# Kernel tuning notes

Hardware: AMD Instinct MI355X
Metric: run time of the kernel (lower is better)

The kernel has to match this reference:

```python
import jax, jax.numpy as jnp
import numpy as np

EMBED_DIM = 512
NUM_HEADS = 8
HEAD_DIM = EMBED_DIM // NUM_HEADS
FACTOR = 5
B, T = 4, 2048


def setup_inputs() -> dict:
    key = jax.random.key(0)
    ks = jax.random.split(key, 10)
    s = EMBED_DIM ** -0.5
    hidden_states = jax.random.normal(ks[0], (B, T, EMBED_DIM), dtype=jnp.float32)
    log_L = int(np.ceil(np.log1p(T)))
    u_part = min(FACTOR * T * log_L, T)
    index_sample = jax.random.randint(ks[1], (u_part,), 0, T, dtype=jnp.int32)
    Wq = jax.random.normal(ks[2], (EMBED_DIM, EMBED_DIM), dtype=jnp.float32) * s
    bq = jnp.zeros((EMBED_DIM,), dtype=jnp.float32)
    Wk = jax.random.normal(ks[3], (EMBED_DIM, EMBED_DIM), dtype=jnp.float32) * s
    bk = jnp.zeros((EMBED_DIM,), dtype=jnp.float32)
    Wv = jax.random.normal(ks[4], (EMBED_DIM, EMBED_DIM), dtype=jnp.float32) * s
    bv = jnp.zeros((EMBED_DIM,), dtype=jnp.float32)
    Wo = jax.random.normal(ks[5], (EMBED_DIM, EMBED_DIM), dtype=jnp.float32) * s
    bo = jnp.zeros((EMBED_DIM,), dtype=jnp.float32)
    return {"hidden_states": hidden_states, "index_sample": index_sample,
            "Wq": Wq, "bq": bq, "Wk": Wk, "bk": bk, "Wv": Wv, "bv": bv,
            "Wo": Wo, "bo": bo}


def _split_heads(x, bsz, seqlen):
    # [B, T, E] -> [B*H, T, head_dim]
    return x.reshape(bsz, seqlen, NUM_HEADS, HEAD_DIM).transpose(0, 2, 1, 3).reshape(bsz * NUM_HEADS, seqlen, HEAD_DIM)


def reference(hidden_states, index_sample, Wq, bq, Wk, bk, Wv, bv, Wo, bo):
    bsz, tgt_len, embed_dim = hidden_states.shape
    scaling = HEAD_DIM ** -0.5
    q = (hidden_states @ Wq.T + bq) * scaling
    k = hidden_states @ Wk.T + bk
    v = hidden_states @ Wv.T + bv
    q = _split_heads(q, bsz, tgt_len)   # [BH, T, d]
    k = _split_heads(k, bsz, tgt_len)
    v = _split_heads(v, bsz, tgt_len)
    L_k = tgt_len
    log_q = int(np.ceil(np.log1p(tgt_len)))
    u = min(FACTOR * log_q, tgt_len)
    # random key sampling (indices precomputed, length u_part)
    k_sample = k[:, index_sample, :]                                  # [BH, u_part, d]
    qk_sample = jnp.einsum('bqd,bkd->bqk', q, k_sample)               # [BH, T, u_part]
    # sparsity measurement: max - mean over sampled keys (mean uses full L_k as in source)
    sparsity = qk_sample.max(axis=-1) - qk_sample.sum(axis=-1) / L_k  # [BH, T]
    top_idx = jax.lax.top_k(sparsity, u)[1]                           # [BH, u]
    q_reduce = jnp.take_along_axis(q, top_idx[:, :, None], axis=1)    # [BH, u, d]
    attn = jax.nn.softmax(jnp.einsum('bud,bkd->buk', q_reduce, k), axis=-1)  # [BH, u, L]
    attn_out = jnp.einsum('buk,bkd->bud', attn, v)                    # [BH, u, d]
    # encoder context: mean of values over time, scattered with active-query outputs
    context = jnp.broadcast_to(v.mean(axis=1, keepdims=True), v.shape)  # [BH, T, d]
    bh_idx = jnp.arange(bsz * NUM_HEADS)[:, None]
    context = context.at[bh_idx, top_idx].set(attn_out)
    out = context.reshape(bsz, NUM_HEADS, tgt_len, HEAD_DIM).transpose(0, 2, 1, 3).reshape(bsz, tgt_len, embed_dim)
    return out @ Wo.T + bo
```

## Files before the change

kernel.cpp:

```cpp
#include <hip/hip_runtime.h>
#include <hip/hip_bf16.h>
#include <math.h>

#define T_LEN 2048
#define EMB   512
#define NHEAD 8
#define HDIM  64
#define BHEADS 32
#define USEL  40

typedef __bf16 bf16v8 __attribute__((ext_vector_type(8)));
typedef _Float16 f16x8 __attribute__((ext_vector_type(8)));
typedef float f32x4 __attribute__((ext_vector_type(4)));
typedef unsigned short u16;

__device__ __forceinline__ void cvt4_hilo(const float4 f, uint2& ph, uint2& pl)
{
    __hip_bfloat16 h0 = __float2bfloat16(f.x);
    __hip_bfloat16 h1 = __float2bfloat16(f.y);
    __hip_bfloat16 h2 = __float2bfloat16(f.z);
    __hip_bfloat16 h3 = __float2bfloat16(f.w);
    __hip_bfloat16 l0 = __float2bfloat16(f.x - __bfloat162float(h0));
    __hip_bfloat16 l1 = __float2bfloat16(f.y - __bfloat162float(h1));
    __hip_bfloat16 l2 = __float2bfloat16(f.z - __bfloat162float(h2));
    __hip_bfloat16 l3 = __float2bfloat16(f.w - __bfloat162float(h3));
    ph.x = (unsigned)*(const u16*)&h0 | ((unsigned)*(const u16*)&h1 << 16);
    ph.y = (unsigned)*(const u16*)&h2 | ((unsigned)*(const u16*)&h3 << 16);
    pl.x = (unsigned)*(const u16*)&l0 | ((unsigned)*(const u16*)&l1 << 16);
    pl.y = (unsigned)*(const u16*)&l2 | ((unsigned)*(const u16*)&l3 << 16);
}

__device__ __forceinline__ void cvt4_hilo_h(const float4 f, uint2& ph, uint2& pl)
{
    _Float16 h0 = (_Float16)f.x;
    _Float16 h1 = (_Float16)f.y;
    _Float16 h2 = (_Float16)f.z;
    _Float16 h3 = (_Float16)f.w;
    _Float16 l0 = (_Float16)(f.x - (float)h0);
    _Float16 l1 = (_Float16)(f.y - (float)h1);
    _Float16 l2 = (_Float16)(f.z - (float)h2);
    _Float16 l3 = (_Float16)(f.w - (float)h3);
    ph.x = (unsigned)*(const u16*)&h0 | ((unsigned)*(const u16*)&h1 << 16);
    ph.y = (unsigned)*(const u16*)&h2 | ((unsigned)*(const u16*)&h3 << 16);
    pl.x = (unsigned)*(const u16*)&l0 | ((unsigned)*(const u16*)&l1 << 16);
    pl.y = (unsigned)*(const u16*)&l2 | ((unsigned)*(const u16*)&l3 << 16);
}

__global__ __launch_bounds__(256)
void pack_hilo_kernel(const float* __restrict__ X,
                      const float* __restrict__ Wq, const float* __restrict__ Wk,
                      const float* __restrict__ Wv,
                      u16* __restrict__ Xp, u16* __restrict__ Wp)
{
    alignas(16) __shared__ u16 th[4096];
    alignas(16) __shared__ u16 tl[4096];
    const int b = blockIdx.x, tid = threadIdx.x;

    const float* src; u16* dst;
    if (b < 1024) {
        int mt = b >> 4, kt = b & 15;
        src = X + (size_t)(mt * 128) * EMB + kt * 32;
        dst = Xp + (size_t)b * 8192;
    } else {
        int wdx = b - 1024;
        int z = wdx >> 6, nt = (wdx >> 4) & 3, kt = wdx & 15;
        const float* W = (z == 0) ? Wq : (z == 1) ? Wk : Wv;
        src = W + (size_t)(nt * 128) * EMB + kt * 32;
        dst = Wp + (size_t)wdx * 8192;
    }

    #pragma unroll
    for (int s = 0; s < 4; ++s) {
        int u = tid + 256 * s;
        int row = u >> 3, c4 = u & 7;
        float4 f = *(const float4*)&src[(size_t)row * EMB + c4 * 4];
        uint2 ph, pl;
        cvt4_hilo_h(f, ph, pl);
        int kq = c4 >> 1, e4 = (c4 & 1) * 4;
        *(uint2*)&th[kq * 1024 + row * 8 + e4] = ph;
        *(uint2*)&tl[kq * 1024 + row * 8 + e4] = pl;
    }
    __syncthreads();

    uint4* d4 = (uint4*)dst;
    const uint4* s4h = (const uint4*)th;
    const uint4* s4l = (const uint4*)tl;
    d4[tid]       = s4h[tid];
    d4[tid + 256] = s4h[tid + 256];
    d4[tid + 512] = s4l[tid];
    d4[tid + 768] = s4l[tid + 256];
}

__global__ __launch_bounds__(256)
void qkv_mfma_kernel(const u16* __restrict__ Xp, const u16* __restrict__ Wp,
                     const float* __restrict__ bq, const float* __restrict__ bk,
                     const float* __restrict__ bv,
                     float* __restrict__ qo, float* __restrict__ ko, float* __restrict__ vo)
{
    alignas(16) __shared__ u16 Ah[2][4096];
    alignas(16) __shared__ u16 Al[2][4096];
    alignas(16) __shared__ u16 Bh[2][4096];
    alignas(16) __shared__ u16 Bl[2][4096];

    const int z = blockIdx.z;
    const float* bias; float* dst; float scale;
    if (z == 0)      { bias = bq; dst = qo; scale = 0.125f; }
    else if (z == 1) { bias = bk; dst = ko; scale = 1.0f;   }
    else             { bias = bv; dst = vo; scale = 1.0f;   }
    const bool three = (z != 2);

    const int tid = threadIdx.x;
    const int mt = blockIdx.x;
    const int nt = blockIdx.y;
    const int w = tid >> 6, lane = tid & 63;
    const int wm = w & 1, wn = w >> 1;
    const int lm = lane & 15, kq = lane >> 4;

    const u16* Abase = Xp + (size_t)mt * (16 * 8192);
    const u16* Bbase = Wp + (size_t)(z * 4 + nt) * (16 * 8192);

    f32x4 acc[4][4];
    #pragma unroll
    for (int i = 0; i < 4; ++i)
        #pragma unroll
        for (int j = 0; j < 4; ++j)
            #pragma unroll
            for (int r = 0; r < 4; ++r) acc[i][j][r] = 0.0f;

    auto stage = [&](int kt, int buf) {
        const u16* at = Abase + kt * 8192;
        const u16* bt = Bbase + kt * 8192;
        const u16* gsrc; u16* ldst;
        if (w == 0)      { gsrc = at;        ldst = &Ah[buf][0]; }
        else if (w == 1) { gsrc = at + 4096; ldst = &Al[buf][0]; }
        else if (w == 2) { gsrc = bt;        ldst = &Bh[buf][0]; }
        else             { gsrc = bt + 4096; ldst = &Bl[buf][0]; }
        if (three || (w & 1) == 0) {
            #pragma unroll
            for (int i = 0; i < 8; ++i)
                __builtin_amdgcn_global_load_lds(
                    (const __attribute__((address_space(1))) void*)(gsrc + (size_t)lane * 8 + i * 512),
                    (__attribute__((address_space(3))) void*)(ldst + i * 512),
                    16, 0, 0);
        }
    };

    stage(0, 0);

    for (int kt = 0; kt < 16; ++kt) {
        const int cur = kt & 1;
        if (kt + 1 < 16) {
            stage(kt + 1, cur ^ 1);
            asm volatile("s_waitcnt vmcnt(8)" ::: "memory");
        } else {
            asm volatile("s_waitcnt vmcnt(0)" ::: "memory");
        }
        __builtin_amdgcn_s_barrier();
        __builtin_amdgcn_sched_barrier(0);

        f16x8 ah[4], al[4], bh[4], bl[4];
        #pragma unroll
        for (int i = 0; i < 4; ++i) {
            int ar = (wm * 64 + i * 16 + lm) * 8 + kq * 1024;
            int br = (wn * 64 + i * 16 + lm) * 8 + kq * 1024;
            ah[i] = *(const f16x8*)&Ah[cur][ar];
            bh[i] = *(const f16x8*)&Bh[cur][br];
            if (three) {
                al[i] = *(const f16x8*)&Al[cur][ar];
                bl[i] = *(const f16x8*)&Bl[cur][br];
            }
        }
        #pragma unroll
        for (int i = 0; i < 4; ++i)
            #pragma unroll
            for (int j = 0; j < 4; ++j) {
                acc[i][j] = __builtin_amdgcn_mfma_f32_16x16x32_f16(ah[i], bh[j], acc[i][j], 0, 0, 0);
                if (three) {
                    acc[i][j] = __builtin_amdgcn_mfma_f32_16x16x32_f16(ah[i], bl[j], acc[i][j], 0, 0, 0);
                    acc[i][j] = __builtin_amdgcn_mfma_f32_16x16x32_f16(al[i], bh[j], acc[i][j], 0, 0, 0);
                }
            }
        __builtin_amdgcn_s_barrier();
    }

    #pragma unroll
    for (int j = 0; j < 4; ++j) {
        int ng = nt * 128 + wn * 64 + j * 16 + lm;
        int h = ng >> 6, d = ng & 63;
        float bv_ = bias[ng];
        #pragma unroll
        for (int i = 0; i < 4; ++i) {
            #pragma unroll
            for (int r = 0; r < 4; ++r) {
                int mg = mt * 128 + wm * 64 + i * 16 + kq * 4 + r;
                int b = mg >> 11, t = mg & 2047;
                dst[((size_t)((b * NHEAD + h) * T_LEN + t)) * HDIM + d] =
                    (acc[i][j][r] + bv_) * scale;
            }
        }
    }
}

__global__ __launch_bounds__(256)
void qkv_proj_kernel(const float* __restrict__ X,
                     const float* __restrict__ Wq, const float* __restrict__ bq,
                     const float* __restrict__ Wk, const float* __restrict__ bk,
                     const float* __restrict__ Wv, const float* __restrict__ bv,
                     float* __restrict__ qo, float* __restrict__ ko, float* __restrict__ vo)
{
    alignas(16) __shared__ u16 Ah[128 * 40];
    alignas(16) __shared__ u16 Al[128 * 40];
    alignas(16) __shared__ u16 Bh[128 * 40];
    alignas(16) __shared__ u16 Bl[128 * 40];

    const int z = blockIdx.z;
    const float* W; const float* bias; float* dst; float scale;
    if (z == 0)      { W = Wq; bias = bq; dst = qo; scale = 0.125f; }
    else if (z == 1) { W = Wk; bias = bk; dst = ko; scale = 1.0f;   }
    else             { W = Wv; bias = bv; dst = vo; scale = 1.0f;   }

    const int tid = threadIdx.x;
    const int m0 = blockIdx.x * 128;
    const int n0 = blockIdx.y * 128;
    const int w = tid >> 6, lane = tid & 63;
    const int wm = w & 1, wn = w >> 1;
    const int lm = lane & 15, kq = lane >> 4;

    f32x4 acc[4][4];
    #pragma unroll
    for (int i = 0; i < 4; ++i)
        #pragma unroll
        for (int j = 0; j < 4; ++j)
            #pragma unroll
            for (int r = 0; r < 4; ++r) acc[i][j][r] = 0.0f;

    for (int kc = 0; kc < EMB; kc += 32) {
        __syncthreads();
        #pragma unroll
        for (int s = 0; s < 4; ++s) {
            int u = tid + 256 * s;
            int row = u >> 3, c4 = u & 7;
            float4 fa = *(const float4*)&X[(size_t)(m0 + row) * EMB + kc + c4 * 4];
            float4 fb = *(const float4*)&W[(n0 + row) * EMB + kc + c4 * 4];
            uint2 ph, pl;
            cvt4_hilo_h(fa, ph, pl);
            *(uint2*)&Ah[row * 40 + c4 * 4] = ph;
            *(uint2*)&Al[row * 40 + c4 * 4] = pl;
            cvt4_hilo_h(fb, ph, pl);
            *(uint2*)&Bh[row * 40 + c4 * 4] = ph;
            *(uint2*)&Bl[row * 40 + c4 * 4] = pl;
        }
        __syncthreads();

        f16x8 ah[4], al[4], bh[4], bl[4];
        #pragma unroll
        for (int i = 0; i < 4; ++i) {
            int ra = (wm * 64 + i * 16 + lm) * 40 + kq * 8;
            ah[i] = *(const f16x8*)&Ah[ra];
            al[i] = *(const f16x8*)&Al[ra];
            int rb = (wn * 64 + i * 16 + lm) * 40 + kq * 8;
            bh[i] = *(const f16x8*)&Bh[rb];
            bl[i] = *(const f16x8*)&Bl[rb];
        }
        #pragma unroll
        for (int i = 0; i < 4; ++i)
            #pragma unroll
            for (int j = 0; j < 4; ++j) {
                acc[i][j] = __builtin_amdgcn_mfma_f32_16x16x32_f16(ah[i], bh[j], acc[i][j], 0, 0, 0);
                acc[i][j] = __builtin_amdgcn_mfma_f32_16x16x32_f16(ah[i], bl[j], acc[i][j], 0, 0, 0);
                acc[i][j] = __builtin_amdgcn_mfma_f32_16x16x32_f16(al[i], bh[j], acc[i][j], 0, 0, 0);
            }
    }

    #pragma unroll
    for (int j = 0; j < 4; ++j) {
        int ng = n0 + wn * 64 + j * 16 + lm;
        int h = ng >> 6, d = ng & 63;
        float bv_ = bias[ng];
        #pragma unroll
        for (int i = 0; i < 4; ++i) {
            #pragma unroll
            for (int r = 0; r < 4; ++r) {
                int mg = m0 + wm * 64 + i * 16 + kq * 4 + r;
                int b = mg >> 11, t = mg & 2047;
                dst[((size_t)((b * NHEAD + h) * T_LEN + t)) * HDIM + d] =
                    (acc[i][j][r] + bv_) * scale;
            }
        }
    }
}

__global__ __launch_bounds__(256)
void count_compact_kernel(const int* __restrict__ idxs, int n,
                          int* __restrict__ count, int* __restrict__ klist,
                          int* __restrict__ ncp)
{
    __shared__ int cnt[T_LEN];
    __shared__ int th_tot[256];
    __shared__ int th_off[256];
    __shared__ int ncs;
    const int tid = threadIdx.x;
    for (int j = tid; j < T_LEN; j += 256) cnt[j] = 0;
    __syncthreads();
    for (int i = tid; i < n; i += 256) atomicAdd(&cnt[idxs[i] & (T_LEN - 1)], 1);
    __syncthreads();
    const int base = tid * 8;
    int flags[8]; int loc = 0;
    #pragma unroll
    for (int j = 0; j < 8; ++j) {
        int c = cnt[base + j];
        count[base + j] = c;
        flags[j] = (c > 0); loc += flags[j];
    }
    th_tot[tid] = loc;
    __syncthreads();
    if (tid == 0) {
        int run = 0;
        for (int i = 0; i < 256; ++i) { th_off[i] = run; run += th_tot[i]; }
        ncs = run;
        ncp[0] = run;
    }
    __syncthreads();
    int off = th_off[tid];
    #pragma unroll
    for (int j = 0; j < 8; ++j)
        if (flags[j]) klist[off++] = base + j;
    __syncthreads();
    const int nc = ncs;
    const int nt = (nc + 127) & ~127;
    const int k0 = klist[0];
    for (int j = nc + tid; j < nt; j += 256) klist[j] = k0;
}

__global__ __launch_bounds__(256)
void ksum_vmean_part_kernel(const int* __restrict__ count,
                            const float* __restrict__ k, const float* __restrict__ v,
                            float* __restrict__ kpart, float* __restrict__ vpart)
{
    __shared__ int cs[256];
    alignas(16) __shared__ float rk[16 * 64];
    alignas(16) __shared__ float rv[16 * 64];

    const int sl = blockIdx.x, bh = blockIdx.y, tid = threadIdx.x;
    const int f4 = tid & 15, tg = tid >> 4;
    const int t0 = sl * 256;

    cs[tid] = count[t0 + tid];
    __syncthreads();

    const float4* k4 = (const float4*)(k + (size_t)bh * T_LEN * HDIM) + t0 * 16;
    const float4* v4 = (const float4*)(v + (size_t)bh * T_LEN * HDIM) + t0 * 16;

    float4 ak = {0.f, 0.f, 0.f, 0.f}, av = {0.f, 0.f, 0.f, 0.f};
    #pragma unroll
    for (int s = 0; s < 16; ++s) {
        int t = tg + s * 16;
        float c = (float)cs[t];
        float4 kf = k4[t * 16 + f4];
        float4 vf = v4[t * 16 + f4];
        ak.x = fmaf(c, kf.x, ak.x); ak.y = fmaf(c, kf.y, ak.y);
        ak.z = fmaf(c, kf.z, ak.z); ak.w = fmaf(c, kf.w, ak.w);
        av.x += vf.x; av.y += vf.y; av.z += vf.z; av.w += vf.w;
    }
    *(float4*)&rk[tg * 64 + f4 * 4] = ak;
    *(float4*)&rv[tg * 64 + f4 * 4] = av;
    __syncthreads();

    if (tid < 64) {
        float sk = 0.f, sv = 0.f;
        #pragma unroll
        for (int g = 0; g < 16; ++g) { sk += rk[g * 64 + tid]; sv += rv[g * 64 + tid]; }
        kpart[((size_t)bh * 8 + sl) * 64 + tid] = sk;
        vpart[((size_t)bh * 8 + sl) * 64 + tid] = sv;
    }
}

__global__ __launch_bounds__(64)
void ksum_vmean_reduce_kernel(const float* __restrict__ kpart, const float* __restrict__ vpart,
                              float* __restrict__ ksum, float* __restrict__ vmean)
{
    const int bh = blockIdx.x, d = threadIdx.x;
    float sk = 0.f, sv = 0.f;
    #pragma unroll
    for (int sl = 0; sl < 8; ++sl) {
        sk += kpart[((size_t)bh * 8 + sl) * 64 + d];
        sv += vpart[((size_t)bh * 8 + sl) * 64 + d];
    }
    ksum[bh * 64 + d]  = sk;
    vmean[bh * 64 + d] = sv * (1.0f / 2048.0f);
}

__global__ __launch_bounds__(256)
void pack_k_kernel(const float* __restrict__ k, const int* __restrict__ klist,
                   const int* __restrict__ ncp, u16* __restrict__ Kp)
{
    alignas(16) __shared__ u16 th[8192];
    alignas(16) __shared__ u16 tl[8192];
    const int wg = blockIdx.x, tid = threadIdx.x;
    const int swz = (wg & 7) * 64 + (wg >> 3);
    const int bh = swz >> 4, kt = swz & 15;
    const int ntiles = (ncp[0] + 127) >> 7;
    if (kt >= ntiles) return;

    const float4* kb4 = (const float4*)(k + (size_t)bh * T_LEN * HDIM);
    #pragma unroll
    for (int s = 0; s < 8; ++s) {
        int u = tid + 256 * s;
        int row = u >> 4, c4 = u & 15;
        int krow = klist[kt * 128 + row];
        float4 f = kb4[krow * 16 + c4];
        uint2 ph, pl;
        cvt4_hilo_h(f, ph, pl);
        int base = (c4 >> 3) * 4096 + ((c4 >> 1) & 3) * 1024 + row * 8 + (c4 & 1) * 4;
        *(uint2*)&th[base] = ph;
        *(uint2*)&tl[base] = pl;
    }
    __syncthreads();

    u16* dst = Kp + ((size_t)bh * 16 + kt) * 16384;
    uint4* d4 = (uint4*)dst;
    const uint4* s4h = (const uint4*)th;
    const uint4* s4l = (const uint4*)tl;
    #pragma unroll
    for (int i = 0; i < 4; ++i) d4[tid + 256 * i] = s4h[tid + 256 * i];
    #pragma unroll
    for (int i = 0; i < 4; ++i) d4[1024 + tid + 256 * i] = s4l[tid + 256 * i];
}

__global__ __launch_bounds__(256)
void sparsity_scan_kernel(const float* __restrict__ q, const u16* __restrict__ Kp,
                          const float* __restrict__ ksum,
                          const int* __restrict__ ncp, float* __restrict__ spars)
{
    alignas(16) __shared__ u16 KH[10240];
    alignas(16) __shared__ u16 KL[10240];
    __shared__ float ksm[64];
    __shared__ float smax[128];
    __shared__ float sdotL[128];

    const int tid = threadIdx.x;
    const int wg = blockIdx.x;
    const int swz = (wg & 7) * 64 + (wg >> 3);
    const int bh = swz >> 4;
    const int q0 = (swz & 15) * 128;
    const int w = tid >> 6, lane = tid & 63;
    const int lm = lane & 15, kq = lane >> 4;

    const float* qb = q + ((size_t)bh * T_LEN + q0) * HDIM;
    const int ntiles = (ncp[0] + 127) >> 7;

    if (tid < 64) ksm[tid] = ksum[bh * 64 + tid];

    #pragma unroll
    for (int s = 0; s < 8; ++s) {
        int u = tid + 256 * s;
        int row = u >> 4, c4 = u & 15;
        float4 f = *(const float4*)&qb[row * HDIM + c4 * 4];
        uint2 ph, pl;
        cvt4_hilo_h(f, ph, pl);
        int base = ((c4 >> 3) * 128 + row) * 40 + (c4 & 7) * 4;
        *(uint2*)&KH[base] = ph;
        *(uint2*)&KL[base] = pl;
    }
    __syncthreads();

    f16x8 qh[2][2], ql[2][2];
    #pragma unroll
    for (int i = 0; i < 2; ++i)
        #pragma unroll
        for (int c = 0; c < 2; ++c) {
            int ra = (c * 128 + w * 32 + i * 16 + lm) * 40 + kq * 8;
            qh[i][c] = *(const f16x8*)&KH[ra];
            ql[i][c] = *(const f16x8*)&KL[ra];
        }

    {
        float4 k0a = *(const float4*)&ksm[kq * 8];
        float4 k0b = *(const float4*)&ksm[kq * 8 + 4];
        float4 k1a = *(const float4*)&ksm[32 + kq * 8];
        float4 k1b = *(const float4*)&ksm[32 + kq * 8 + 4];
        float kmv[2][8] = {{k0a.x, k0a.y, k0a.z, k0a.w, k0b.x, k0b.y, k0b.z, k0b.w},
                           {k1a.x, k1a.y, k1a.z, k1a.w, k1b.x, k1b.y, k1b.z, k1b.w}};
        #pragma unroll
        for (int i = 0; i < 2; ++i) {
            float sd = 0.f;
            #pragma unroll
            for (int c = 0; c < 2; ++c)
                #pragma unroll
                for (int e = 0; e < 8; ++e)
                    sd = fmaf((float)qh[i][c][e] + (float)ql[i][c][e], kmv[c][e], sd);
            sd += __shfl_xor(sd, 16, 64);
            sd += __shfl_xor(sd, 32, 64);
            if (kq == 0) sdotL[w * 32 + i * 16 + lm] = sd;
        }
    }

    float vmax[2][4];
    #pragma unroll
    for (int i = 0; i < 2; ++i)
        #pragma unroll
        for (int r = 0; r < 4; ++r) vmax[i][r] = -INFINITY;

    const u16* kpb = Kp + (size_t)bh * (16 * 16384);

    for (int kt = 0; kt < ntiles; ++kt) {
        __syncthreads();
        const u16* kp = kpb + kt * 16384;
        const u16* gsrc; u16* ldst;
        if (w == 0)      { gsrc = kp;         ldst = KH; }
        else if (w == 1) { gsrc = kp + 4096;  ldst = KH + 4096; }
        else if (w == 2) { gsrc = kp + 8192;  ldst = KL; }
        else             { gsrc = kp + 12288; ldst = KL + 4096; }
        #pragma unroll
        for (int i = 0; i < 8; ++i)
            __builtin_amdgcn_global_load_lds(
                (const __attribute__((address_space(1))) void*)(gsrc + (size_t)lane * 8 + i * 512),
                (__attribute__((address_space(3))) void*)(ldst + i * 512),
                16, 0, 0);
        __syncthreads();

        #pragma unroll
        for (int j = 0; j < 8; ++j) {
            int rb0 = kq * 1024 + (j * 16 + lm) * 8;
            int rb1 = 4096 + kq * 1024 + (j * 16 + lm) * 8;
            f16x8 bh0 = *(const f16x8*)&KH[rb0];
            f16x8 bl0 = *(const f16x8*)&KL[rb0];
            f16x8 bh1 = *(const f16x8*)&KH[rb1];
            f16x8 bl1 = *(const f16x8*)&KL[rb1];
            f32x4 a0 = {0.f, 0.f, 0.f, 0.f};
            f32x4 a1 = {0.f, 0.f, 0.f, 0.f};
            a0 = __builtin_amdgcn_mfma_f32_16x16x32_f16(qh[0][0], bh0, a0, 0, 0, 0);
            a1 = __builtin_amdgcn_mfma_f32_16x16x32_f16(qh[1][0], bh0, a1, 0, 0, 0);
            a0 = __builtin_amdgcn_mfma_f32_16x16x32_f16(qh[0][0], bl0, a0, 0, 0, 0);
            a1 = __builtin_amdgcn_mfma_f32_16x16x32_f16(qh[1][0], bl0, a1, 0, 0, 0);
            a0 = __builtin_amdgcn_mfma_f32_16x16x32_f16(ql[0][0], bh0, a0, 0, 0, 0);
            a1 = __builtin_amdgcn_mfma_f32_16x16x32_f16(ql[1][0], bh0, a1, 0, 0, 0);
            a0 = __builtin_amdgcn_mfma_f32_16x16x32_f16(qh[0][1], bh1, a0, 0, 0, 0);
            a1 = __builtin_amdgcn_mfma_f32_16x16x32_f16(qh[1][1], bh1, a1, 0, 0, 0);
            a0 = __builtin_amdgcn_mfma_f32_16x16x32_f16(qh[0][1], bl1, a0, 0, 0, 0);
            a1 = __builtin_amdgcn_mfma_f32_16x16x32_f16(qh[1][1], bl1, a1, 0, 0, 0);
            a0 = __builtin_amdgcn_mfma_f32_16x16x32_f16(ql[0][1], bh1, a0, 0, 0, 0);
            a1 = __builtin_amdgcn_mfma_f32_16x16x32_f16(ql[1][1], bh1, a1, 0, 0, 0);
            #pragma unroll
            for (int r = 0; r < 4; ++r) {
                vmax[0][r] = fmaxf(vmax[0][r], a0[r]);
                vmax[1][r] = fmaxf(vmax[1][r], a1[r]);
            }
        }
    }

    #pragma unroll
    for (int i = 0; i < 2; ++i)
        #pragma unroll
        for (int r = 0; r < 4; ++r) {
            float m = vmax[i][r];
            m = fmaxf(m, __shfl_xor(m, 1, 64));
            m = fmaxf(m, __shfl_xor(m, 2, 64));
            m = fmaxf(m, __shfl_xor(m, 4, 64));
            m = fmaxf(m, __shfl_xor(m, 8, 64));
            if (lm == 0) smax[w * 32 + i * 16 + kq * 4 + r] = m;
        }
    __syncthreads();

    if (tid < 128)
        spars[bh * T_LEN + q0 + tid] = smax[tid] - sdotL[tid] * (1.0f / 2048.0f);
}

__global__ __launch_bounds__(256)
void sparsity_scan_fb_kernel(const float* __restrict__ q, const float* __restrict__ k,
                             const float* __restrict__ ksum, const int* __restrict__ klist,
                             const int* __restrict__ ncp, float* __restrict__ spars)
{
    alignas(16) __shared__ u16 KH[256 * 40];
    alignas(16) __shared__ u16 KL[256 * 40];
    __shared__ float ksm[64];
    __shared__ float smax[128];
    __shared__ float sdotL[128];

    const int tid = threadIdx.x;
    const int bh = blockIdx.y;
    const int q0 = blockIdx.x * 128;
    const int w = tid >> 6, lane = tid & 63;
    const int lm = lane & 15, kq = lane >> 4;

    const float* qb = q + ((size_t)bh * T_LEN + q0) * HDIM;
    const float4* kb4 = (const float4*)(k + (size_t)bh * T_LEN * HDIM);
    const int ntiles = (ncp[0] + 127) >> 7;

    if (tid < 64) ksm[tid] = ksum[bh * 64 + tid];

    #pragma unroll
    for (int s = 0; s < 8; ++s) {
        int u = tid + 256 * s;
        int row = u >> 4, c4 = u & 15;
        float4 f = *(const float4*)&qb[row * HDIM + c4 * 4];
        uint2 ph, pl;
        cvt4_hilo_h(f, ph, pl);
        int base = ((c4 >> 3) * 128 + row) * 40 + (c4 & 7) * 4;
        *(uint2*)&KH[base] = ph;
        *(uint2*)&KL[base] = pl;
    }
    __syncthreads();

    f16x8 qh[2][2], ql[2][2];
    #pragma unroll
    for (int i = 0; i < 2; ++i)
        #pragma unroll
        for (int c = 0; c < 2; ++c) {
            int ra = (c * 128 + w * 32 + i * 16 + lm) * 40 + kq * 8;
            qh[i][c] = *(const f16x8*)&KH[ra];
            ql[i][c] = *(const f16x8*)&KL[ra];
        }

    {
        float4 k0a = *(const float4*)&ksm[kq * 8];
        float4 k0b = *(const float4*)&ksm[kq * 8 + 4];
        float4 k1a = *(const float4*)&ksm[32 + kq * 8];
        float4 k1b = *(const float4*)&ksm[32 + kq * 8 + 4];
        float kmv[2][8] = {{k0a.x, k0a.y, k0a.z, k0a.w, k0b.x, k0b.y, k0b.z, k0b.w},
                           {k1a.x, k1a.y, k1a.z, k1a.w, k1b.x, k1b.y, k1b.z, k1b.w}};
        #pragma unroll
        for (int i = 0; i < 2; ++i) {
            float sd = 0.f;
            #pragma unroll
            for (int c = 0; c < 2; ++c)
                #pragma unroll
                for (int e = 0; e < 8; ++e)
                    sd = fmaf((float)qh[i][c][e] + (float)ql[i][c][e], kmv[c][e], sd);
            sd += __shfl_xor(sd, 16, 64);
            sd += __shfl_xor(sd, 32, 64);
            if (kq == 0) sdotL[w * 32 + i * 16 + lm] = sd;
        }
    }

    float vmax[2][4];
    #pragma unroll
    for (int i = 0; i < 2; ++i)
        #pragma unroll
        for (int r = 0; r < 4; ++r) vmax[i][r] = -INFINITY;

    for (int kt = 0; kt < ntiles; ++kt) {
        __syncthreads();
        #pragma unroll
        for (int s = 0; s < 8; ++s) {
            int u = tid + 256 * s;
            int row = u >> 4, c4 = u & 15;
            int krow = klist[kt * 128 + row];
            float4 f = kb4[krow * 16 + c4];
            uint2 ph, pl;
            cvt4_hilo_h(f, ph, pl);
            int base = ((c4 >> 3) * 128 + row) * 40 + (c4 & 7) * 4;
            *(uint2*)&KH[base] = ph;
            *(uint2*)&KL[base] = pl;
        }
        __syncthreads();

        #pragma unroll
        for (int j = 0; j < 8; ++j) {
            int rb0 = (j * 16 + lm) * 40 + kq * 8;
            int rb1 = (128 + j * 16 + lm) * 40 + kq * 8;
            f16x8 bh0 = *(const f16x8*)&KH[rb0];
            f16x8 bl0 = *(const f16x8*)&KL[rb0];
            f16x8 bh1 = *(const f16x8*)&KH[rb1];
            f16x8 bl1 = *(const f16x8*)&KL[rb1];
            f32x4 a0 = {0.f, 0.f, 0.f, 0.f};
            f32x4 a1 = {0.f, 0.f, 0.f, 0.f};
            a0 = __builtin_amdgcn_mfma_f32_16x16x32_f16(qh[0][0], bh0, a0, 0, 0, 0);
            a1 = __builtin_amdgcn_mfma_f32_16x16x32_f16(qh[1][0], bh0, a1, 0, 0, 0);
            a0 = __builtin_amdgcn_mfma_f32_16x16x32_f16(qh[0][0], bl0, a0, 0, 0, 0);
            a1 = __builtin_amdgcn_mfma_f32_16x16x32_f16(qh[1][0], bl0, a1, 0, 0, 0);
            a0 = __builtin_amdgcn_mfma_f32_16x16x32_f16(ql[0][0], bh0, a0, 0, 0, 0);
            a1 = __builtin_amdgcn_mfma_f32_16x16x32_f16(ql[1][0], bh0, a1, 0, 0, 0);
            a0 = __builtin_amdgcn_mfma_f32_16x16x32_f16(qh[0][1], bh1, a0, 0, 0, 0);
            a1 = __builtin_amdgcn_mfma_f32_16x16x32_f16(qh[1][1], bh1, a1, 0, 0, 0);
            a0 = __builtin_amdgcn_mfma_f32_16x16x32_f16(qh[0][1], bl1, a0, 0, 0, 0);
            a1 = __builtin_amdgcn_mfma_f32_16x16x32_f16(qh[1][1], bl1, a1, 0, 0, 0);
            a0 = __builtin_amdgcn_mfma_f32_16x16x32_f16(ql[0][1], bh1, a0, 0, 0, 0);
            a1 = __builtin_amdgcn_mfma_f32_16x16x32_f16(ql[1][1], bh1, a1, 0, 0, 0);
            #pragma unroll
            for (int r = 0; r < 4; ++r) {
                vmax[0][r] = fmaxf(vmax[0][r], a0[r]);
                vmax[1][r] = fmaxf(vmax[1][r], a1[r]);
            }
        }
    }

    #pragma unroll
    for (int i = 0; i < 2; ++i)
        #pragma unroll
        for (int r = 0; r < 4; ++r) {
            float m = vmax[i][r];
            m = fmaxf(m, __shfl_xor(m, 1, 64));
            m = fmaxf(m, __shfl_xor(m, 2, 64));
            m = fmaxf(m, __shfl_xor(m, 4, 64));
            m = fmaxf(m, __shfl_xor(m, 8, 64));
            if (lm == 0) smax[w * 32 + i * 16 + kq * 4 + r] = m;
        }
    __syncthreads();

    if (tid < 128)
        spars[bh * T_LEN + q0 + tid] = smax[tid] - sdotL[tid] * (1.0f / 2048.0f);
}

__global__ __launch_bounds__(256)
void topk_kernel(const float* __restrict__ spars, int* __restrict__ topi)
{
    __shared__ unsigned keys[T_LEN];
    __shared__ int hist[256];
    __shared__ int sfx[257];
    __shared__ int sh_need, sh_bin, nsel, neq, cnt2;
    const int bh = blockIdx.x, tid = threadIdx.x;

    #pragma unroll
    for (int s = 0; s < 8; ++s) {
        int j = tid + 256 * s;
        unsigned u = __float_as_uint(spars[bh * T_LEN + j]);
        keys[j] = (u & 0x80000000u) ? ~u : (u | 0x80000000u);
    }
    if (tid == 0) { sh_need = USEL; nsel = 0; neq = 0; cnt2 = 0; }
    __syncthreads();

    unsigned kpref = 0;
    int shift = 24;
    #pragma unroll
    for (int level = 0; level < 4; ++level) {
        const unsigned hi_mask = (shift == 24) ? 0u : (0xFFFFFFFFu << (shift + 8));
        hist[tid] = 0;
        __syncthreads();
        #pragma unroll
        for (int s = 0; s < 8; ++s) {
            unsigned kk = keys[tid + 256 * s];
            if ((kk & hi_mask) == kpref)
                atomicAdd(&hist[(kk >> shift) & 255], 1);
        }
        __syncthreads();
        sfx[tid] = hist[tid];
        if (tid == 0) sfx[256] = 0;
        __syncthreads();
        for (int off = 1; off < 256; off <<= 1) {
            int v = (tid + off < 256) ? sfx[tid + off] : 0;
            __syncthreads();
            sfx[tid] += v;
            __syncthreads();
        }
        const int need = sh_need;
        const int A = (tid == 255) ? 0 : sfx[tid + 1];
        const int here = sfx[tid];
        __syncthreads();
        if (A < need && here >= need) {
            sh_bin = tid;
            sh_need = need - A;
        }
        __syncthreads();
        kpref |= (unsigned)sh_bin << shift;
        shift -= 8;
    }

    const unsigned K = kpref;
    const int need_eq = sh_need;

    #pragma unroll
    for (int s = 0; s < 8; ++s) {
        int j = tid + 256 * s;
        unsigned kk = keys[j];
        if (kk > K) {
            int pos = atomicAdd(&nsel, 1);
            if (pos < USEL) topi[bh * USEL + pos] = j;
        } else if (kk == K) {
            atomicAdd(&neq, 1);
        }
    }
    __syncthreads();
    const int base = nsel;
    const int E = neq;
    __syncthreads();

    if (E == need_eq) {
        #pragma unroll
        for (int s = 0; s < 8; ++s) {
            int j = tid + 256 * s;
            if (keys[j] == K) {
                int pos = atomicAdd(&cnt2, 1);
                if (base + pos < USEL) topi[bh * USEL + base + pos] = j;
            }
        }
    } else {
        #pragma unroll
        for (int s = 0; s < 8; ++s) {
            int j = tid + 256 * s;
            if (keys[j] == K) {
                int rank = 0;
                for (int j2 = 0; j2 < j; ++j2) rank += (keys[j2] == K);
                if (rank < need_eq && base + rank < USEL)
                    topi[bh * USEL + base + rank] = j;
            }
        }
    }
}

__global__ __launch_bounds__(256)
void gather_q_kernel(const float* __restrict__ q, const int* __restrict__ topi,
                     float* __restrict__ qsel)
{
    const int bh = blockIdx.x, tid = threadIdx.x;
    for (int i = tid; i < USEL * HDIM; i += 256) {
        int u = i >> 6, d = i & 63;
        int t = topi[bh * USEL + u] & (T_LEN - 1);
        qsel[(size_t)bh * USEL * HDIM + i] = q[((size_t)bh * T_LEN + t) * HDIM + d];
    }
}

__global__ __launch_bounds__(256)
void sel_scores_kernel(const float* __restrict__ qsel, const float* __restrict__ k,
                       float* __restrict__ S)
{
    __shared__ float qsT[64 * 41];
    __shared__ float ksT[64 * 257];

    const int sl = blockIdx.x, bh = blockIdx.y, tid = threadIdx.x;
    const int t0 = sl * 256;

    for (int i = tid; i < USEL * HDIM; i += 256) {
        int u = i >> 6, d = i & 63;
        qsT[d * 41 + u] = qsel[(size_t)bh * USEL * HDIM + i];
    }
    const float4* k4 = (const float4*)(k + (size_t)bh * T_LEN * HDIM);
    #pragma unroll
    for (int s = 0; s < 16; ++s) {
        int u = tid + 256 * s;
        int c4 = u & 15, t = u >> 4;
        float4 f = k4[(t0 + t) * 16 + c4];
        ksT[(c4 * 4 + 0) * 257 + t] = f.x;
        ksT[(c4 * 4 + 1) * 257 + t] = f.y;
        ksT[(c4 * 4 + 2) * 257 + t] = f.z;
        ksT[(c4 * 4 + 3) * 257 + t] = f.w;
    }
    __syncthreads();

    const int qg = tid >> 5;
    const int kg = tid & 31;

    float acc[5][8];
    #pragma unroll
    for (int i = 0; i < 5; ++i)
        #pragma unroll
        for (int j = 0; j < 8; ++j) acc[i][j] = 0.0f;

    #pragma unroll 4
    for (int d = 0; d < 64; ++d) {
        float qv[5], kv[8];
        #pragma unroll
        for (int i = 0; i < 5; ++i) qv[i] = qsT[d * 41 + qg * 5 + i];
        #pragma unroll
        for (int j = 0; j < 8; ++j) kv[j] = ksT[d * 257 + kg + 32 * j];
        #pragma unroll
        for (int i = 0; i < 5; ++i)
            #pragma unroll
            for (int j = 0; j < 8; ++j)
                acc[i][j] = fmaf(qv[i], kv[j], acc[i][j]);
    }

    #pragma unroll
    for (int i = 0; i < 5; ++i) {
        float* sp = &S[((size_t)bh * USEL + qg * 5 + i) * T_LEN + t0 + kg];
        #pragma unroll
        for (int j = 0; j < 8; ++j) sp[32 * j] = acc[i][j];
    }
}

__global__ __launch_bounds__(256)
void sel_softmax_kernel(float* __restrict__ S)
{
    __shared__ float red[256];
    const int row = blockIdx.x, tid = threadIdx.x;
    float* sr = S + (size_t)row * T_LEN;

    float x[8];
    float m = -INFINITY;
    #pragma unroll
    for (int s = 0; s < 8; ++s) { x[s] = sr[tid + 256 * s]; m = fmaxf(m, x[s]); }
    red[tid] = m;
    __syncthreads();
    for (int s = 128; s > 0; s >>= 1) {
        if (tid < s) red[tid] = fmaxf(red[tid], red[tid + s]);
        __syncthreads();
    }
    m = red[0];
    __syncthreads();

    float sum = 0.f;
    #pragma unroll
    for (int s = 0; s < 8; ++s) { x[s] = __expf(x[s] - m); sum += x[s]; }
    red[tid] = sum;
    __syncthreads();
    for (int s = 128; s > 0; s >>= 1) {
        if (tid < s) red[tid] += red[tid + s];
        __syncthreads();
    }
    float inv = 1.0f / red[0];
    #pragma unroll
    for (int s = 0; s < 8; ++s) sr[tid + 256 * s] = x[s] * inv;
}

__global__ __launch_bounds__(256)
void pv_part_kernel(const float* __restrict__ S, const float* __restrict__ v,
                    float* __restrict__ part)
{
    __shared__ float ps[USEL * 128];
    __shared__ float vs[128 * 69];
    __shared__ float obuf[128 * 20];

    const int sl = blockIdx.x, bh = blockIdx.y, tid = threadIdx.x;
    const int t0 = sl * 128;

    for (int i = tid; i < USEL * 128; i += 256) {
        int q = i >> 7, t = i & 127;
        ps[q * 128 + t] = S[((size_t)bh * USEL + q) * T_LEN + t0 + t];
    }
    const float4* v4 = (const float4*)(v + (size_t)bh * T_LEN * HDIM);
    #pragma unroll
    for (int s = 0; s < 8; ++s) {
        int u = tid + 256 * s;
        int c4 = u & 15, t = u >> 4;
        float4 f = v4[(t0 + t) * 16 + c4];
        vs[t * 69 + c4 * 4 + 0] = f.x;
        vs[t * 69 + c4 * 4 + 1] = f.y;
        vs[t * 69 + c4 * 4 + 2] = f.z;
        vs[t * 69 + c4 * 4 + 3] = f.w;
    }
    __syncthreads();

    const int qg = tid >> 5, r = tid & 31;
    const int dg = r >> 1, th = r & 1;
    const int tb = th * 64;

    float o[5][4];
    #pragma unroll
    for (int i = 0; i < 5; ++i)
        #pragma unroll
        for (int j = 0; j < 4; ++j) o[i][j] = 0.0f;

    #pragma unroll 4
    for (int tt = 0; tt < 64; ++tt) {
        int t = tb + tt;
        float pv[5];
        #pragma unroll
        for (int i = 0; i < 5; ++i) pv[i] = ps[(qg * 5 + i) * 128 + t];
        float4 vv = *(const float4*)&vs[t * 69 + dg * 4];
        #pragma unroll
        for (int i = 0; i < 5; ++i) {
            o[i][0] = fmaf(pv[i], vv.x, o[i][0]);
            o[i][1] = fmaf(pv[i], vv.y, o[i][1]);
            o[i][2] = fmaf(pv[i], vv.z, o[i][2]);
            o[i][3] = fmaf(pv[i], vv.w, o[i][3]);
        }
    }

    const int p = qg * 16 + dg;
    if (th == 1) {
        #pragma unroll
        for (int i = 0; i < 5; ++i)
            #pragma unroll
            for (int j = 0; j < 4; ++j) obuf[p * 20 + i * 4 + j] = o[i][j];
    }
    __syncthreads();
    if (th == 0) {
        float* pb = part + ((size_t)bh * 16 + sl) * (USEL * HDIM);
        #pragma unroll
        for (int i = 0; i < 5; ++i)
            #pragma unroll
            for (int j = 0; j < 4; ++j)
                pb[(qg * 5 + i) * HDIM + dg * 4 + j] = o[i][j] + obuf[p * 20 + i * 4 + j];
    }
}

__global__ __launch_bounds__(256)
void pv_merge_kernel(const float* __restrict__ part, float* __restrict__ attn)
{
    const int bh = blockIdx.x, tid = threadIdx.x;
    for (int i = tid; i < USEL * HDIM; i += 256) {
        float s = 0.f;
        #pragma unroll
        for (int sl = 0; sl < 16; ++sl)
            s += part[((size_t)bh * 16 + sl) * (USEL * HDIM) + i];
        attn[(size_t)bh * USEL * HDIM + i] = s;
    }
}

__global__ __launch_bounds__(256)
void ctx_fill_kernel(const float* __restrict__ vmean, float* __restrict__ ctx)
{
    int flat = blockIdx.x * 256 + threadIdx.x;
    int d = flat & 63, h = (flat >> 6) & 7, b = flat >> 20;
    int bh = (b << 3) | h;
    ctx[flat] = vmean[bh * 64 + d];
}

__global__ void ctx_scatter_kernel(const float* __restrict__ attn, const int* __restrict__ topi,
                                   float* __restrict__ ctx)
{
    const int u = blockIdx.x, bh = blockIdx.y, d = threadIdx.x;
    const int b = bh >> 3, h = bh & 7;
    const int t = topi[bh * USEL + u] & (T_LEN - 1);
    ctx[(size_t)(b * T_LEN + t) * EMB + h * 64 + d] =
        attn[((size_t)bh * USEL + u) * HDIM + d];
}

__global__ __launch_bounds__(256)
void out_proj_kernel(const float* __restrict__ A, const float* __restrict__ Wo,
                     const float* __restrict__ bo, float* __restrict__ out)
{
    alignas(16) __shared__ u16 Ah[128 * 40];
    alignas(16) __shared__ u16 Al[128 * 40];
    alignas(16) __shared__ u16 Bh[128 * 40];
    alignas(16) __shared__ u16 Bl[128 * 40];

    const int tid = threadIdx.x;
    const int m0 = blockIdx.x * 128;
    const int n0 = blockIdx.y * 128;
    const int w = tid >> 6, lane = tid & 63;
    const int wm = w & 1, wn = w >> 1;
    const int lm = lane & 15, kq = lane >> 4;

    f32x4 acc[4][4];
    #pragma unroll
    for (int i = 0; i < 4; ++i)
        #pragma unroll
        for (int j = 0; j < 4; ++j)
            #pragma unroll
            for (int r = 0; r < 4; ++r) acc[i][j][r] = 0.0f;

    for (int kc = 0; kc < EMB; kc += 32) {
        __syncthreads();
        #pragma unroll
        for (int s = 0; s < 4; ++s) {
            int u = tid + 256 * s;
            int row = u >> 3, c4 = u & 7;
            float4 fa = *(const float4*)&A[(size_t)(m0 + row) * EMB + kc + c4 * 4];
            float4 fb = *(const float4*)&Wo[(n0 + row) * EMB + kc + c4 * 4];
            uint2 ph, pl;
            cvt4_hilo(fa, ph, pl);
            *(uint2*)&Ah[row * 40 + c4 * 4] = ph;
            *(uint2*)&Al[row * 40 + c4 * 4] = pl;
            cvt4_hilo(fb, ph, pl);
            *(uint2*)&Bh[row * 40 + c4 * 4] = ph;
            *(uint2*)&Bl[row * 40 + c4 * 4] = pl;
        }
        __syncthreads();

        bf16v8 ah[4], al[4], bh[4], bl[4];
        #pragma unroll
        for (int i = 0; i < 4; ++i) {
            int ra = (wm * 64 + i * 16 + lm) * 40 + kq * 8;
            ah[i] = *(const bf16v8*)&Ah[ra];
            al[i] = *(const bf16v8*)&Al[ra];
            int rb = (wn * 64 + i * 16 + lm) * 40 + kq * 8;
            bh[i] = *(const bf16v8*)&Bh[rb];
            bl[i] = *(const bf16v8*)&Bl[rb];
        }
        #pragma unroll
        for (int i = 0; i < 4; ++i)
            #pragma unroll
            for (int j = 0; j < 4; ++j) {
                acc[i][j] = __builtin_amdgcn_mfma_f32_16x16x32_bf16(ah[i], bh[j], acc[i][j], 0, 0, 0);
                acc[i][j] = __builtin_amdgcn_mfma_f32_16x16x32_bf16(ah[i], bl[j], acc[i][j], 0, 0, 0);
                acc[i][j] = __builtin_amdgcn_mfma_f32_16x16x32_bf16(al[i], bh[j], acc[i][j], 0, 0, 0);
            }
    }

    #pragma unroll
    for (int j = 0; j < 4; ++j) {
        int ng = n0 + wn * 64 + j * 16 + lm;
        float bias = bo[ng];
        #pragma unroll
        for (int i = 0; i < 4; ++i)
            #pragma unroll
            for (int r = 0; r < 4; ++r) {
                int mg = m0 + wm * 64 + i * 16 + kq * 4 + r;
                out[(size_t)mg * EMB + ng] = acc[i][j][r] + bias;
            }
    }
}

__global__ __launch_bounds__(256)
void ws_diag_kernel(float* __restrict__ out, int n, float mib)
{
    int flat = blockIdx.x * 256 + threadIdx.x;
    if (flat < n) out[flat] = mib;
}

extern "C" void kernel_launch(void* const* d_in, const int* in_sizes, int n_in,
                              void* d_out, int out_size, void* d_ws, size_t ws_size,
                              hipStream_t stream)
{
    const float* X = nullptr; const int* idxs = nullptr;
    const float* Wseen[4] = {nullptr, nullptr, nullptr, nullptr};
    const float* bseen[4] = {nullptr, nullptr, nullptr, nullptr};
    int nw = 0, nb = 0, u_part = 2048;
    for (int i = 0; i < n_in; ++i) {
        int sz = in_sizes[i];
        if (sz == EMB * EMB * 16) { if (!X) X = (const float*)d_in[i]; }
        else if (sz == T_LEN)     { if (!idxs) { idxs = (const int*)d_in[i]; u_part = sz; } }
        else if (sz == EMB * EMB) { if (nw < 4) Wseen[nw++] = (const float*)d_in[i]; }
        else if (sz == EMB)       { if (nb < 4) bseen[nb++] = (const float*)d_in[i]; }
    }
    if (!X || !idxs || nw < 4 || nb < 4) {
        X = (const float*)d_in[0]; idxs = (const int*)d_in[1];
        Wseen[0] = (const float*)d_in[2]; bseen[0] = (const float*)d_in[3];
        Wseen[1] = (const float*)d_in[4]; bseen[1] = (const float*)d_in[5];
        Wseen[2] = (const float*)d_in[6]; bseen[2] = (const float*)d_in[7];
        Wseen[3] = (const float*)d_in[8]; bseen[3] = (const float*)d_in[9];
        u_part = in_sizes[1];
    }
    const float *Wq = Wseen[0], *Wk = Wseen[1], *Wv = Wseen[2], *Wo = Wseen[3];
    const float *bq = bseen[0], *bk = bseen[1], *bv = bseen[2], *bo = bseen[3];

    const size_t NEED      = 50951168ULL;
    const size_t NEED_BIG  = NEED + 16777216ULL + 3145728ULL;
    if (ws_size < NEED) {
        ws_diag_kernel<<<(out_size + 255) / 256, 256, 0, stream>>>(
            (float*)d_out, out_size, (float)(ws_size >> 20));
        return;
    }

    float* ws    = (float*)d_ws;
    float* qw    = ws;
    float* kw    = qw + 4194304;
    float* vw    = kw + 4194304;
    float* tail  = vw + 4194304;
    float* slotA = tail;
    float* spars = tail + 81920;
    int*   count = (int*)(tail + 147456);
    float* ksum  = tail + 149504;
    float* vmean = tail + 151552;
    int*   topi  = (int*)(tail + 153600);
    float* kpart = tail;
    float* vpart = tail + 16384;
    int*   klist = (int*)(tail + 32768);
    int*   ncp   = (int*)(tail + 34816);
    float* S     = qw;
    float* pvp   = qw + 2621440;
    float* qsel  = slotA;
    float* attn  = slotA;
    float* ctx   = (float*)d_ws;
    u16*   Xp    = (u16*)((char*)d_ws + NEED);
    u16*   Wp    = Xp + 8388608;
    u16*   Kp    = Xp;

    const bool big = (ws_size >= NEED_BIG);

    if (big) {
        pack_hilo_kernel<<<1216, 256, 0, stream>>>(X, Wq, Wk, Wv, Xp, Wp);
        qkv_mfma_kernel<<<dim3(64, 4, 3), 256, 0, stream>>>(Xp, Wp, bq, bk, bv, qw, kw, vw);
    } else {
        qkv_proj_kernel<<<dim3(64, 4, 3), 256, 0, stream>>>(X, Wq, bq, Wk, bk, Wv, bv, qw, kw, vw);
    }
    count_compact_kernel<<<1, 256, 0, stream>>>(idxs, u_part, count, klist, ncp);
    ksum_vmean_part_kernel<<<dim3(8, 32), 256, 0, stream>>>(count, kw, vw, kpart, vpart);
    ksum_vmean_reduce_kernel<<<32, 64, 0, stream>>>(kpart, vpart, ksum, vmean);
    if (big) {
        pack_k_kernel<<<512, 256, 0, stream>>>(kw, klist, ncp, Kp);
        sparsity_scan_kernel<<<512, 256, 0, stream>>>(qw, Kp, ksum, ncp, spars);
    } else {
        sparsity_scan_fb_kernel<<<dim3(16, 32), 256, 0, stream>>>(qw, kw, ksum, klist, ncp, spars);
    }
    topk_kernel<<<32, 256, 0, stream>>>(spars, topi);
    gather_q_kernel<<<32, 256, 0, stream>>>(qw, topi, qsel);
    sel_scores_kernel<<<dim3(8, 32), 256, 0, stream>>>(qsel, kw, S);
    sel_softmax_kernel<<<1280, 256, 0, stream>>>(S);
    pv_part_kernel<<<dim3(16, 32), 256, 0, stream>>>(S, vw, pvp);
    pv_merge_kernel<<<32, 256, 0, stream>>>(pvp, attn);
    ctx_fill_kernel<<<16384, 256, 0, stream>>>(vmean, ctx);
    ctx_scatter_kernel<<<dim3(USEL, BHEADS), 64, 0, stream>>>(attn, topi, ctx);
    out_proj_kernel<<<dim3(64, 4), 256, 0, stream>>>(ctx, Wo, bo, (float*)d_out);
}
```

Measured before the change: 277.0 us.

## Run output projection on split-fp16 MFMA with pre-packed context tiles

```diff
diff --git a/kernel.cpp b/kernel.cpp
--- a/kernel.cpp
+++ b/kernel.cpp
@@ -46,10 +46,18 @@
     pl.y = (unsigned)*(const u16*)&l2 | ((unsigned)*(const u16*)&l3 << 16);
 }
 
+__device__ __forceinline__ void cvt1_hilo_h(float f, u16& h, u16& l)
+{
+    _Float16 hh = (_Float16)f;
+    _Float16 ll = (_Float16)(f - (float)hh);
+    h = *(const u16*)&hh;
+    l = *(const u16*)&ll;
+}
+
 __global__ __launch_bounds__(256)
 void pack_hilo_kernel(const float* __restrict__ X,
                       const float* __restrict__ Wq, const float* __restrict__ Wk,
-                      const float* __restrict__ Wv,
+                      const float* __restrict__ Wv, const float* __restrict__ Wo,
                       u16* __restrict__ Xp, u16* __restrict__ Wp)
 {
     alignas(16) __shared__ u16 th[4096];
@@ -64,7 +72,7 @@
     } else {
         int wdx = b - 1024;
         int z = wdx >> 6, nt = (wdx >> 4) & 3, kt = wdx & 15;
-        const float* W = (z == 0) ? Wq : (z == 1) ? Wk : Wv;
+        const float* W = (z == 0) ? Wq : (z == 1) ? Wk : (z == 2) ? Wv : Wo;
         src = W + (size_t)(nt * 128) * EMB + kt * 32;
         dst = Wp + (size_t)wdx * 8192;
     }
@@ -988,6 +996,152 @@
 }
 
 __global__ __launch_bounds__(256)
+void ctx_fill_pack_kernel(const float* __restrict__ vmean, u16* __restrict__ CXp)
+{
+    const int tile = blockIdx.x;
+    const int tid = threadIdx.x;
+    const int mt = tile >> 4, kt = tile & 15;
+    const int bh = ((mt >> 4) << 3) | (kt >> 1);
+    const int dbase = (kt & 1) * 32;
+
+    uint4 vh[4], vl[4];
+    #pragma unroll
+    for (int kq = 0; kq < 4; ++kq) {
+        unsigned hw[4], lw[4];
+        #pragma unroll
+        for (int p = 0; p < 4; ++p) {
+            u16 h0, l0, h1, l1;
+            cvt1_hilo_h(vmean[bh * 64 + dbase + kq * 8 + p * 2],     h0, l0);
+            cvt1_hilo_h(vmean[bh * 64 + dbase + kq * 8 + p * 2 + 1], h1, l1);
+            hw[p] = (unsigned)h0 | ((unsigned)h1 << 16);
+            lw[p] = (unsigned)l0 | ((unsigned)l1 << 16);
+        }
+        vh[kq] = make_uint4(hw[0], hw[1], hw[2], hw[3]);
+        vl[kq] = make_uint4(lw[0], lw[1], lw[2], lw[3]);
+    }
+
+    u16* dst = CXp + (size_t)tile * 8192;
+    uint4* dh = (uint4*)dst;
+    uint4* dl = (uint4*)(dst + 4096);
+    #pragma unroll
+    for (int s = 0; s < 2; ++s) {
+        int u = tid + 256 * s;
+        dh[u] = vh[u >> 7];
+        dl[u] = vl[u >> 7];
+    }
+}
+
+__global__ void ctx_scatter_pack_kernel(const float* __restrict__ attn,
+                                        const int* __restrict__ topi,
+                                        u16* __restrict__ CXp)
+{
+    const int u = blockIdx.x, bh = blockIdx.y, d = threadIdx.x;
+    const int b = bh >> 3, h = bh & 7;
+    const int t = topi[bh * USEL + u] & (T_LEN - 1);
+    const int m = b * T_LEN + t;
+    const int mt = m >> 7, row = m & 127;
+    const int e = h * 64 + d;
+    const int kt = e >> 5;
+    const int c = e & 31, kq = c >> 3, i = c & 7;
+    u16 hh, ll;
+    cvt1_hilo_h(attn[((size_t)bh * USEL + u) * HDIM + d], hh, ll);
+    u16* base = CXp + (size_t)(mt * 16 + kt) * 8192 + kq * 1024 + row * 8 + i;
+    base[0]    = hh;
+    base[4096] = ll;
+}
+
+__global__ __launch_bounds__(256)
+void out_mfma_kernel(const u16* __restrict__ CXp, const u16* __restrict__ Wp,
+                     const float* __restrict__ bo, float* __restrict__ out)
+{
+    alignas(16) __shared__ u16 Ah[2][4096];
+    alignas(16) __shared__ u16 Al[2][4096];
+    alignas(16) __shared__ u16 Bh[2][4096];
+    alignas(16) __shared__ u16 Bl[2][4096];
+
+    const int tid = threadIdx.x;
+    const int mt = blockIdx.x;
+    const int nt = blockIdx.y;
+    const int w = tid >> 6, lane = tid & 63;
+    const int wm = w & 1, wn = w >> 1;
+    const int lm = lane & 15, kq = lane >> 4;
+
+    const u16* Abase = CXp + (size_t)mt * (16 * 8192);
+    const u16* Bbase = Wp + (size_t)(3 * 4 + nt) * (16 * 8192);
+
+    f32x4 acc[4][4];
+    #pragma unroll
+    for (int i = 0; i < 4; ++i)
+        #pragma unroll
+        for (int j = 0; j < 4; ++j)
+            #pragma unroll
+            for (int r = 0; r < 4; ++r) acc[i][j][r] = 0.0f;
+
+    auto stage = [&](int kt, int buf) {
+        const u16* at = Abase + kt * 8192;
+        const u16* bt = Bbase + kt * 8192;
+        const u16* gsrc; u16* ldst;
+        if (w == 0)      { gsrc = at;        ldst = &Ah[buf][0]; }
+        else if (w == 1) { gsrc = at + 4096; ldst = &Al[buf][0]; }
+        else if (w == 2) { gsrc = bt;        ldst = &Bh[buf][0]; }
+        else             { gsrc = bt + 4096; ldst = &Bl[buf][0]; }
+        #pragma unroll
+        for (int i = 0; i < 8; ++i)
+            __builtin_amdgcn_global_load_lds(
+                (const __attribute__((address_space(1))) void*)(gsrc + (size_t)lane * 8 + i * 512),
+                (__attribute__((address_space(3))) void*)(ldst + i * 512),
+                16, 0, 0);
+    };
+
+    stage(0, 0);
+
+    for (int kt = 0; kt < 16; ++kt) {
+        const int cur = kt & 1;
+        if (kt + 1 < 16) {
+            stage(kt + 1, cur ^ 1);
+            asm volatile("s_waitcnt vmcnt(8)" ::: "memory");
+        } else {
+            asm volatile("s_waitcnt vmcnt(0)" ::: "memory");
+        }
+        __builtin_amdgcn_s_barrier();
+        __builtin_amdgcn_sched_barrier(0);
+
+        f16x8 ah[4], al[4], bh[4], bl[4];
+        #pragma unroll
+        for (int i = 0; i < 4; ++i) {
+            int ar = (wm * 64 + i * 16 + lm) * 8 + kq * 1024;
+            int br = (wn * 64 + i * 16 + lm) * 8 + kq * 1024;
+            ah[i] = *(const f16x8*)&Ah[cur][ar];
+            al[i] = *(const f16x8*)&Al[cur][ar];
+            bh[i] = *(const f16x8*)&Bh[cur][br];
+            bl[i] = *(const f16x8*)&Bl[cur][br];
+        }
+        #pragma unroll
+        for (int i = 0; i < 4; ++i)
+            #pragma unroll
+            for (int j = 0; j < 4; ++j) {
+                acc[i][j] = __builtin_amdgcn_mfma_f32_16x16x32_f16(ah[i], bh[j], acc[i][j], 0, 0, 0);
+                acc[i][j] = __builtin_amdgcn_mfma_f32_16x16x32_f16(ah[i], bl[j], acc[i][j], 0, 0, 0);
+                acc[i][j] = __builtin_amdgcn_mfma_f32_16x16x32_f16(al[i], bh[j], acc[i][j], 0, 0, 0);
+            }
+        __builtin_amdgcn_s_barrier();
+    }
+
+    #pragma unroll
+    for (int j = 0; j < 4; ++j) {
+        int ng = nt * 128 + wn * 64 + j * 16 + lm;
+        float bias = bo[ng];
+        #pragma unroll
+        for (int i = 0; i < 4; ++i)
+            #pragma unroll
+            for (int r = 0; r < 4; ++r) {
+                int mg = mt * 128 + wm * 64 + i * 16 + kq * 4 + r;
+                out[(size_t)mg * EMB + ng] = acc[i][j][r] + bias;
+            }
+    }
+}
+
+__global__ __launch_bounds__(256)
 void ctx_fill_kernel(const float* __restrict__ vmean, float* __restrict__ ctx)
 {
     int flat = blockIdx.x * 256 + threadIdx.x;
@@ -1116,7 +1270,10 @@
     const float *bq = bseen[0], *bk = bseen[1], *bv = bseen[2], *bo = bseen[3];
 
     const size_t NEED      = 50951168ULL;
-    const size_t NEED_BIG  = NEED + 16777216ULL + 3145728ULL;
+    const size_t XP_B      = 16777216ULL;
+    const size_t WP_B      = 4194304ULL;
+    const size_t CXP_B     = 16777216ULL;
+    const size_t NEED_BIG  = NEED + XP_B + WP_B + CXP_B;
     if (ws_size < NEED) {
         ws_diag_kernel<<<(out_size + 255) / 256, 256, 0, stream>>>(
             (float*)d_out, out_size, (float)(ws_size >> 20));
@@ -1144,13 +1301,14 @@
     float* attn  = slotA;
     float* ctx   = (float*)d_ws;
     u16*   Xp    = (u16*)((char*)d_ws + NEED);
-    u16*   Wp    = Xp + 8388608;
+    u16*   Wp    = (u16*)((char*)d_ws + NEED + XP_B);
+    u16*   CXp   = (u16*)((char*)d_ws + NEED + XP_B + WP_B);
     u16*   Kp    = Xp;
 
     const bool big = (ws_size >= NEED_BIG);
 
     if (big) {
-        pack_hilo_kernel<<<1216, 256, 0, stream>>>(X, Wq, Wk, Wv, Xp, Wp);
+        pack_hilo_kernel<<<1280, 256, 0, stream>>>(X, Wq, Wk, Wv, Wo, Xp, Wp);
         qkv_mfma_kernel<<<dim3(64, 4, 3), 256, 0, stream>>>(Xp, Wp, bq, bk, bv, qw, kw, vw);
     } else {
         qkv_proj_kernel<<<dim3(64, 4, 3), 256, 0, stream>>>(X, Wq, bq, Wk, bk, Wv, bv, qw, kw, vw);
@@ -1170,7 +1328,13 @@
     sel_softmax_kernel<<<1280, 256, 0, stream>>>(S);
     pv_part_kernel<<<dim3(16, 32), 256, 0, stream>>>(S, vw, pvp);
     pv_merge_kernel<<<32, 256, 0, stream>>>(pvp, attn);
-    ctx_fill_kernel<<<16384, 256, 0, stream>>>(vmean, ctx);
-    ctx_scatter_kernel<<<dim3(USEL, BHEADS), 64, 0, stream>>>(attn, topi, ctx);
-    out_proj_kernel<<<dim3(64, 4), 256, 0, stream>>>(ctx, Wo, bo, (float*)d_out);
-}
+    if (big) {
+        ctx_fill_pack_kernel<<<1024, 256, 0, stream>>>(vmean, CXp);
+        ctx_scatter_pack_kernel<<<dim3(USEL, BHEADS), 64, 0, stream>>>(attn, topi, CXp);
+        out_mfma_kernel<<<dim3(64, 4), 256, 0, stream>>>(CXp, Wp, bo, (float*)d_out);
+    } else {
+        ctx_fill_kernel<<<16384, 256, 0, stream>>>(vmean, ctx);
+        ctx_scatter_kernel<<<dim3(USEL, BHEADS), 64, 0, stream>>>(attn, topi, ctx);
+        out_proj_kernel<<<dim3(64, 4), 256, 0, stream>>>(ctx, Wo, bo, (float*)d_out);
+    }
+}
```

Result: no change. 274.1 us (-1.1%).
